# Optimization experiments

Hardware: AMD Instinct MI355X
Metric: run time of the kernel (lower is better)

Reference implementation:

```python
import jax, jax.numpy as jnp
import numpy as np

TOKENS = 8192
MODEL_DIM = 4096
PROMPT_DIM = 64
NUM_EXPERTS = 8
TOP_K = 2
EPS = float(np.finfo(np.float32).eps)


def setup_inputs() -> dict:
    key = jax.random.key(0)
    k1, k2, k3 = jax.random.split(key, 3)
    x = jax.random.normal(k1, (TOKENS, MODEL_DIM), dtype=jnp.float32)
    prompt = jax.random.normal(k2, (TOKENS, PROMPT_DIM), dtype=jnp.float32)
    # gate linear: Linear(model_dim + prompt_dim, num_experts, bias=True)
    W = jax.random.normal(k3, (MODEL_DIM + PROMPT_DIM, NUM_EXPERTS), dtype=jnp.float32) * 0.02
    b = jnp.zeros((NUM_EXPERTS,), dtype=jnp.float32)
    return {"x": x, "prompt": prompt, "W": W, "b": b}


def reference(x, prompt, W, b):
    # eval path: no jitter, no noise (self.training is False)
    logits = jnp.concatenate([x, prompt], axis=-1) @ W + b          # [T, E]
    _, topk_idx = jax.lax.top_k(logits, TOP_K)                      # [T, K]
    masks = jax.nn.one_hot(topk_idx, NUM_EXPERTS, dtype=jnp.float32)  # [T, K, E]
    gates = jax.nn.softmax(logits, axis=-1)                         # [T, E]
    gates_s = jnp.einsum("te,tke->tk", gates, masks)               # masked gather-sum
    if TOP_K > 1:
        denom = jnp.maximum(gates_s.sum(axis=-1, keepdims=True), EPS)
        gates_s = gates_s / denom
    # masks[:, i] == masks_se[i], gates_s[:, i] == gates_s[i] in the torch code
    return masks, gates_s
```

## Files before the change

kernel.cpp:

```cpp
#include <hip/hip_runtime.h>
#include <math.h>

#define NE 8
#define KDIM 4096
#define PDIM 64
#define WROWS (KDIM + PDIM)
#define EPS_F32 1.1920929e-07f
#define NCHUNK 16
#define DEPTH 3
#define WPB 4
#define TPW 4

typedef float f4 __attribute__((ext_vector_type(4)));

__global__ __launch_bounds__(256)
void transpose_w(const float* __restrict__ W, float* __restrict__ Wt) {
    const int k = blockIdx.x * 256 + threadIdx.x;
    if (k < WROWS) {
        float v[NE];
#pragma unroll
        for (int e = 0; e < NE; ++e) v[e] = W[(size_t)k * NE + e];
#pragma unroll
        for (int e = 0; e < NE; ++e) Wt[(size_t)e * WROWS + k] = v[e];
    }
}

__global__ __launch_bounds__(256, 2)
void topk_gate(const float* __restrict__ x,
               const float* __restrict__ prompt,
               const float* __restrict__ Wt,
               const float* __restrict__ b,
               float* __restrict__ out,
               int tokens)
{
    const int tid   = threadIdx.x;
    const int lane  = tid & 63;
    const int wid   = tid >> 6;
    const int tbase = (blockIdx.x * WPB + wid) * TPW;
    const int klane = lane * 4;
    const int phase = (blockIdx.x * 5) & 15;

    float acc[TPW][NE];
#pragma unroll
    for (int t = 0; t < TPW; ++t)
#pragma unroll
        for (int e = 0; e < NE; ++e) acc[t][e] = 0.f;

    const f4* xp[TPW];
#pragma unroll
    for (int t = 0; t < TPW; ++t)
        xp[t] = (const f4*)(x + (size_t)(tbase + t) * KDIM + klane);
    const f4* wp[NE];
#pragma unroll
    for (int e = 0; e < NE; ++e)
        wp[e] = (const f4*)(Wt + (size_t)e * WROWS + klane);

    f4 xb[DEPTH][TPW];
    f4 wb[DEPTH][NE];

    auto load_chunk = [&](int c, int s) {
        const int coff = ((c + phase) & 15) * 64;
#pragma unroll
        for (int t = 0; t < TPW; ++t)
            xb[s][t] = xp[t][coff];
#pragma unroll
        for (int e = 0; e < NE; ++e)
            wb[s][e] = wp[e][coff];
    };

    load_chunk(0, 0);
    load_chunk(1, 1);

#pragma unroll
    for (int c = 0; c < NCHUNK; ++c) {
        if (c + 2 < NCHUNK) load_chunk(c + 2, (c + 2) % DEPTH);
        const int s = c % DEPTH;
#pragma unroll
        for (int t = 0; t < TPW; ++t)
#pragma unroll
            for (int e = 0; e < NE; ++e) {
                acc[t][e] = fmaf(xb[s][t].x, wb[s][e].x, acc[t][e]);
                acc[t][e] = fmaf(xb[s][t].y, wb[s][e].y, acc[t][e]);
                acc[t][e] = fmaf(xb[s][t].z, wb[s][e].z, acc[t][e]);
                acc[t][e] = fmaf(xb[s][t].w, wb[s][e].w, acc[t][e]);
            }
    }

    if (lane < 16) {
        const int k = lane * 4;
        f4 pv[TPW];
#pragma unroll
        for (int t = 0; t < TPW; ++t)
            pv[t] = *(const f4*)(prompt + (size_t)(tbase + t) * PDIM + k);
        f4 wv[NE];
#pragma unroll
        for (int e = 0; e < NE; ++e)
            wv[e] = *(const f4*)(Wt + (size_t)e * WROWS + KDIM + k);
#pragma unroll
        for (int t = 0; t < TPW; ++t)
#pragma unroll
            for (int e = 0; e < NE; ++e) {
                acc[t][e] = fmaf(pv[t].x, wv[e].x, acc[t][e]);
                acc[t][e] = fmaf(pv[t].y, wv[e].y, acc[t][e]);
                acc[t][e] = fmaf(pv[t].z, wv[e].z, acc[t][e]);
                acc[t][e] = fmaf(pv[t].w, wv[e].w, acc[t][e]);
            }
    }

#pragma unroll
    for (int t = 0; t < TPW; ++t)
#pragma unroll
        for (int e = 0; e < NE; ++e) {
            float v = acc[t][e];
#pragma unroll
            for (int off = 32; off >= 1; off >>= 1)
                v += __shfl_xor(v, off, 64);
            acc[t][e] = v;
        }

    const int tt = lane >> 4;
    const int kk = (lane >> 3) & 1;
    const int ee = lane & 7;

    float lg[NE];
#pragma unroll
    for (int e = 0; e < NE; ++e) {
        float v = acc[0][e];
        if (tt == 1) v = acc[1][e];
        if (tt == 2) v = acc[2][e];
        if (tt == 3) v = acc[3][e];
        lg[e] = v + b[e];
    }

    float v0 = lg[0]; int i0 = 0;
#pragma unroll
    for (int e = 1; e < NE; ++e)
        if (lg[e] > v0) { v0 = lg[e]; i0 = e; }
    float v1 = (i0 == 0) ? lg[1] : lg[0];
    int   i1 = (i0 == 0) ? 1 : 0;
#pragma unroll
    for (int e = 0; e < NE; ++e)
        if (e != i0 && lg[e] > v1) { v1 = lg[e]; i1 = e; }

    float s = 0.f;
#pragma unroll
    for (int e = 0; e < NE; ++e) s += __expf(lg[e] - v0);
    const float g0 = 1.0f / s;
    const float g1 = __expf(v1 - v0) / s;
    const float denom = fmaxf(g0 + g1, EPS_F32);

    const int sel = kk ? i1 : i0;
    const int t_global = tbase + tt;
    out[(size_t)t_global * 16 + kk * 8 + ee] = (ee == sel) ? 1.0f : 0.0f;

    if ((lane & 15) < 2) {
        const float g = (ee == 0) ? (g0 / denom) : (g1 / denom);
        out[(size_t)tokens * 16 + (size_t)t_global * 2 + ee] = g;
    }
}

extern "C" void kernel_launch(void* const* d_in, const int* in_sizes, int n_in,
                              void* d_out, int out_size, void* d_ws, size_t ws_size,
                              hipStream_t stream) {
    const float* x      = (const float*)d_in[0];
    const float* prompt = (const float*)d_in[1];
    const float* W      = (const float*)d_in[2];
    const float* b      = (const float*)d_in[3];
    float* out          = (float*)d_out;
    float* Wt           = (float*)d_ws;

    const int tokens = in_sizes[0] / KDIM;

    hipLaunchKernelGGL(transpose_w, dim3((WROWS + 255) / 256), dim3(256), 0, stream,
                       W, Wt);
    hipLaunchKernelGGL(topk_gate, dim3(tokens / (WPB * TPW)), dim3(256), 0, stream,
                       x, prompt, Wt, b, out, tokens);
}
```

Baseline: 235.6 us.

## Use single-wave blocks with two tokens per wave and asymmetric prefetch buffers

Restructures the gating kernel so each 64-thread block handles two tokens instead of four waves each handling four tokens. This launches twice as many waves and lowers per-thread register use to improve occupancy and latency hiding on the memory-bound x stream. The W prefetch depth drops to double-buffering while x keeps triple-buffering. In exchange, each loaded W chunk is reused across fewer tokens, so L2/W traffic rises.

```diff
diff --git a/kernel.cpp b/kernel.cpp
--- a/kernel.cpp
+++ b/kernel.cpp
@@ -7,9 +7,7 @@
 #define WROWS (KDIM + PDIM)
 #define EPS_F32 1.1920929e-07f
 #define NCHUNK 16
-#define DEPTH 3
-#define WPB 4
-#define TPW 4
+#define TPW 2
 
 typedef float f4 __attribute__((ext_vector_type(4)));
 
@@ -25,7 +23,7 @@
     }
 }
 
-__global__ __launch_bounds__(256, 2)
+__global__ __launch_bounds__(64, 4)
 void topk_gate(const float* __restrict__ x,
                const float* __restrict__ prompt,
                const float* __restrict__ Wt,
@@ -33,10 +31,8 @@
                float* __restrict__ out,
                int tokens)
 {
-    const int tid   = threadIdx.x;
-    const int lane  = tid & 63;
-    const int wid   = tid >> 6;
-    const int tbase = (blockIdx.x * WPB + wid) * TPW;
+    const int lane  = threadIdx.x;
+    const int tbase = blockIdx.x * TPW;
     const int klane = lane * 4;
     const int phase = (blockIdx.x * 5) & 15;
 
@@ -46,43 +42,55 @@
 #pragma unroll
         for (int e = 0; e < NE; ++e) acc[t][e] = 0.f;
 
-    const f4* xp[TPW];
-#pragma unroll
-    for (int t = 0; t < TPW; ++t)
-        xp[t] = (const f4*)(x + (size_t)(tbase + t) * KDIM + klane);
-    const f4* wp[NE];
+    const float* xr0 = x + (size_t)tbase * KDIM;
+    const float* xr1 = xr0 + KDIM;
+    const float* wr[NE];
 #pragma unroll
     for (int e = 0; e < NE; ++e)
-        wp[e] = (const f4*)(Wt + (size_t)e * WROWS + klane);
+        wr[e] = Wt + (size_t)e * WROWS;
 
-    f4 xb[DEPTH][TPW];
-    f4 wb[DEPTH][NE];
+    f4 xb[3][TPW];
+    f4 wb[2][NE];
 
-    auto load_chunk = [&](int c, int s) {
-        const int coff = ((c + phase) & 15) * 64;
-#pragma unroll
-        for (int t = 0; t < TPW; ++t)
-            xb[s][t] = xp[t][coff];
+    auto koff = [&](int c) { return ((c + phase) & 15) * 256 + klane; };
+
+    {
+        const int k0 = koff(0);
 #pragma unroll
         for (int e = 0; e < NE; ++e)
-            wb[s][e] = wp[e][coff];
-    };
-
-    load_chunk(0, 0);
-    load_chunk(1, 1);
+            wb[0][e] = *(const f4*)(wr[e] + k0);
+        xb[0][0] = *(const f4*)(xr0 + k0);
+        xb[0][1] = *(const f4*)(xr1 + k0);
+        const int k1 = koff(1);
+        xb[1][0] = *(const f4*)(xr0 + k1);
+        xb[1][1] = *(const f4*)(xr1 + k1);
+    }
 
 #pragma unroll
     for (int c = 0; c < NCHUNK; ++c) {
-        if (c + 2 < NCHUNK) load_chunk(c + 2, (c + 2) % DEPTH);
-        const int s = c % DEPTH;
+        if (c + 1 < NCHUNK) {
+            const int kw = koff(c + 1);
+#pragma unroll
+            for (int e = 0; e < NE; ++e)
+                wb[(c + 1) & 1][e] = *(const f4*)(wr[e] + kw);
+        }
+        if (c + 2 < NCHUNK) {
+            const int kx = koff(c + 2);
+            xb[(c + 2) % 3][0] = *(const f4*)(xr0 + kx);
+            xb[(c + 2) % 3][1] = *(const f4*)(xr1 + kx);
+        }
+
+        const int s = c % 3;
+        const int wv = c & 1;
 #pragma unroll
         for (int t = 0; t < TPW; ++t)
 #pragma unroll
             for (int e = 0; e < NE; ++e) {
-                acc[t][e] = fmaf(xb[s][t].x, wb[s][e].x, acc[t][e]);
-                acc[t][e] = fmaf(xb[s][t].y, wb[s][e].y, acc[t][e]);
-                acc[t][e] = fmaf(xb[s][t].z, wb[s][e].z, acc[t][e]);
-                acc[t][e] = fmaf(xb[s][t].w, wb[s][e].w, acc[t][e]);
+                const f4 xv = xb[s][t];
+                acc[t][e] = fmaf(xv.x, wb[wv][e].x, acc[t][e]);
+                acc[t][e] = fmaf(xv.y, wb[wv][e].y, acc[t][e]);
+                acc[t][e] = fmaf(xv.z, wb[wv][e].z, acc[t][e]);
+                acc[t][e] = fmaf(xv.w, wb[wv][e].w, acc[t][e]);
             }
     }
 
@@ -92,19 +100,17 @@
 #pragma unroll
         for (int t = 0; t < TPW; ++t)
             pv[t] = *(const f4*)(prompt + (size_t)(tbase + t) * PDIM + k);
-        f4 wv[NE];
 #pragma unroll
-        for (int e = 0; e < NE; ++e)
-            wv[e] = *(const f4*)(Wt + (size_t)e * WROWS + KDIM + k);
+        for (int e = 0; e < NE; ++e) {
+            const f4 wv = *(const f4*)(Wt + (size_t)e * WROWS + KDIM + k);
 #pragma unroll
-        for (int t = 0; t < TPW; ++t)
-#pragma unroll
-            for (int e = 0; e < NE; ++e) {
-                acc[t][e] = fmaf(pv[t].x, wv[e].x, acc[t][e]);
-                acc[t][e] = fmaf(pv[t].y, wv[e].y, acc[t][e]);
-                acc[t][e] = fmaf(pv[t].z, wv[e].z, acc[t][e]);
-                acc[t][e] = fmaf(pv[t].w, wv[e].w, acc[t][e]);
+            for (int t = 0; t < TPW; ++t) {
+                acc[t][e] = fmaf(pv[t].x, wv.x, acc[t][e]);
+                acc[t][e] = fmaf(pv[t].y, wv.y, acc[t][e]);
+                acc[t][e] = fmaf(pv[t].z, wv.z, acc[t][e]);
+                acc[t][e] = fmaf(pv[t].w, wv.w, acc[t][e]);
             }
+        }
     }
 
 #pragma unroll
@@ -118,17 +124,14 @@
             acc[t][e] = v;
         }
 
-    const int tt = lane >> 4;
+    const int tt = (lane >> 4) & 1;
     const int kk = (lane >> 3) & 1;
     const int ee = lane & 7;
 
     float lg[NE];
 #pragma unroll
     for (int e = 0; e < NE; ++e) {
-        float v = acc[0][e];
-        if (tt == 1) v = acc[1][e];
-        if (tt == 2) v = acc[2][e];
-        if (tt == 3) v = acc[3][e];
+        const float v = (tt == 0) ? acc[0][e] : acc[1][e];
         lg[e] = v + b[e];
     }
 
@@ -149,13 +152,15 @@
     const float g1 = __expf(v1 - v0) / s;
     const float denom = fmaxf(g0 + g1, EPS_F32);
 
-    const int sel = kk ? i1 : i0;
-    const int t_global = tbase + tt;
-    out[(size_t)t_global * 16 + kk * 8 + ee] = (ee == sel) ? 1.0f : 0.0f;
+    if (lane < 32) {
+        const int sel = kk ? i1 : i0;
+        const int t_global = tbase + tt;
+        out[(size_t)t_global * 16 + kk * 8 + ee] = (ee == sel) ? 1.0f : 0.0f;
 
-    if ((lane & 15) < 2) {
-        const float g = (ee == 0) ? (g0 / denom) : (g1 / denom);
-        out[(size_t)tokens * 16 + (size_t)t_global * 2 + ee] = g;
+        if ((lane & 15) < 2) {
+            const float g = (ee == 0) ? (g0 / denom) : (g1 / denom);
+            out[(size_t)tokens * 16 + (size_t)t_global * 2 + ee] = g;
+        }
     }
 }
 
@@ -173,6 +178,6 @@
 
     hipLaunchKernelGGL(transpose_w, dim3((WROWS + 255) / 256), dim3(256), 0, stream,
                        W, Wt);
-    hipLaunchKernelGGL(topk_gate, dim3(tokens / (WPB * TPW)), dim3(256), 0, stream,
+    hipLaunchKernelGGL(topk_gate, dim3(tokens / TPW), dim3(64), 0, stream,
                        x, prompt, Wt, b, out, tokens);
 }
```

Measured after the change: 215.6 us. 8.5% less time.
